# Kernel tuning notes

Measured on AMD Instinct MI355X. Metric: run time of the kernel, lower is better.

The kernel has to match this reference:

```python
import jax, jax.numpy as jnp
import numpy as np

CLAMP_MIN = 1e-12
CLAMP_MAX = 1e12


def setup_inputs() -> dict:
    key = jax.random.key(0)
    k1, k2, k3 = jax.random.split(key, 3)
    B, C, D = 16384, 751, 2048
    x = jax.random.normal(k1, (B, D), dtype=jnp.float32)
    labels = jax.random.randint(k2, (B,), 0, C, dtype=jnp.int64)
    centers = jax.random.normal(k3, (C, D), dtype=jnp.float32)
    return {"x": x, "labels": labels, "centers": centers}


def reference(x, labels, centers):
    # Original builds a full (B, C) squared-distance matrix and then, per row,
    # boolean-masks out the entry at column labels[i]. Mathematically that is
    # just the squared distance between x[i] and centers[labels[i]]; gradients
    # also only flow through those gathered entries, so we gather directly.
    c = centers[labels]                       # (B, D) own-class centers
    dist = (jnp.sum(x * x, axis=1)
            + jnp.sum(c * c, axis=1)
            - 2.0 * jnp.sum(x * c, axis=1))   # (B,) squared distances
    dist = jnp.clip(dist, CLAMP_MIN, CLAMP_MAX)
    return jnp.mean(dist)
```

## Files before the change

kernel.cpp:

```cpp
#include <hip/hip_runtime.h>

constexpr int B = 16384;
constexpr int D = 2048;
constexpr float CLAMP_MIN = 1e-12f;
constexpr float CLAMP_MAX = 1e12f;

constexpr int GRID1  = 2048;
constexpr int BLOCK1 = 256;

__global__ __launch_bounds__(BLOCK1) void center_loss_pass1(
    const float* __restrict__ x,
    const int* __restrict__ labels,
    const float* __restrict__ centers,
    float* __restrict__ partials)
{
    const int lane            = threadIdx.x & 63;
    const int wave_in_block   = threadIdx.x >> 6;
    const int waves_per_block = BLOCK1 >> 6;
    const int global_wave     = blockIdx.x * waves_per_block + wave_in_block;
    const int num_waves       = GRID1 * waves_per_block;

    float acc = 0.0f;

    for (int row = global_wave; row < B; row += num_waves) {
        const int lbl = __builtin_amdgcn_readfirstlane(labels[row]);
        const float4* __restrict__ xr =
            reinterpret_cast<const float4*>(x + (size_t)row * D);
        const float4* __restrict__ cr =
            reinterpret_cast<const float4*>(centers + (size_t)lbl * D);

        float partial = 0.0f;
        #pragma unroll
        for (int j = 0; j < D / 4 / 64; ++j) {
            float4 xv = xr[j * 64 + lane];
            float4 cv = cr[j * 64 + lane];
            float d0 = xv.x - cv.x;
            float d1 = xv.y - cv.y;
            float d2 = xv.z - cv.z;
            float d3 = xv.w - cv.w;
            partial = fmaf(d0, d0,
                      fmaf(d1, d1,
                      fmaf(d2, d2,
                      fmaf(d3, d3, partial))));
        }

        #pragma unroll
        for (int off = 32; off > 0; off >>= 1)
            partial += __shfl_xor(partial, off, 64);

        if (lane == 0) {
            acc += fminf(fmaxf(partial, CLAMP_MIN), CLAMP_MAX);
        }
    }

    __shared__ float s[4];
    if (lane == 0) s[wave_in_block] = acc;
    __syncthreads();
    if (threadIdx.x == 0) {
        partials[blockIdx.x] = (s[0] + s[1]) + (s[2] + s[3]);
    }
}

__global__ __launch_bounds__(256) void center_loss_pass2(
    const float* __restrict__ partials,
    float* __restrict__ out)
{
    const int tid = threadIdx.x;
    float v = 0.0f;
    #pragma unroll
    for (int j = 0; j < GRID1 / 256; ++j)
        v += partials[j * 256 + tid];

    #pragma unroll
    for (int off = 32; off > 0; off >>= 1)
        v += __shfl_xor(v, off, 64);

    __shared__ float s[4];
    if ((tid & 63) == 0) s[tid >> 6] = v;
    __syncthreads();
    if (tid == 0)
        out[0] = ((s[0] + s[1]) + (s[2] + s[3])) * (1.0f / (float)B);
}

extern "C" void kernel_launch(void* const* d_in, const int* in_sizes, int n_in,
                              void* d_out, int out_size, void* d_ws, size_t ws_size,
                              hipStream_t stream) {
    const float* x       = (const float*)d_in[0];
    const int*   labels  = (const int*)d_in[1];
    const float* centers = (const float*)d_in[2];
    float*       out     = (float*)d_out;
    float*       partials = (float*)d_ws;

    center_loss_pass1<<<GRID1, BLOCK1, 0, stream>>>(x, labels, centers, partials);
    center_loss_pass2<<<1, 256, 0, stream>>>(partials, out);
}
```

Before: 194.5 us.

## Fuse two-pass reduction into one cooperative kernel with grid sync

Merges the partial-sum kernel and the final reduction kernel into one cooperative launch that uses a grid-wide barrier, removing the second kernel launch. It halves the grid to 1024 blocks so all blocks can be co-resident, and marks x loads as nontemporal so the streamed data does not evict reused center rows from cache. The cost is grid-sync overhead and fewer waves available to hide memory latency.

```diff
diff --git a/kernel.cpp b/kernel.cpp
--- a/kernel.cpp
+++ b/kernel.cpp
@@ -1,18 +1,24 @@
 #include <hip/hip_runtime.h>
+#include <hip/hip_cooperative_groups.h>
+
+namespace cg = cooperative_groups;
 
 constexpr int B = 16384;
 constexpr int D = 2048;
 constexpr float CLAMP_MIN = 1e-12f;
 constexpr float CLAMP_MAX = 1e12f;
 
-constexpr int GRID1  = 2048;
+constexpr int GRID1  = 1024;
 constexpr int BLOCK1 = 256;
 
-__global__ __launch_bounds__(BLOCK1) void center_loss_pass1(
+typedef float vfloat4 __attribute__((ext_vector_type(4)));
+
+__global__ __launch_bounds__(BLOCK1, 4) void center_loss_coop(
     const float* __restrict__ x,
     const int* __restrict__ labels,
     const float* __restrict__ centers,
-    float* __restrict__ partials)
+    float* __restrict__ partials,
+    float* __restrict__ out)
 {
     const int lane            = threadIdx.x & 63;
     const int wave_in_block   = threadIdx.x >> 6;
@@ -24,16 +30,16 @@
 
     for (int row = global_wave; row < B; row += num_waves) {
         const int lbl = __builtin_amdgcn_readfirstlane(labels[row]);
-        const float4* __restrict__ xr =
-            reinterpret_cast<const float4*>(x + (size_t)row * D);
-        const float4* __restrict__ cr =
-            reinterpret_cast<const float4*>(centers + (size_t)lbl * D);
+        const vfloat4* __restrict__ xr =
+            reinterpret_cast<const vfloat4*>(x + (size_t)row * D);
+        const vfloat4* __restrict__ cr =
+            reinterpret_cast<const vfloat4*>(centers + (size_t)lbl * D);
 
         float partial = 0.0f;
         #pragma unroll
         for (int j = 0; j < D / 4 / 64; ++j) {
-            float4 xv = xr[j * 64 + lane];
-            float4 cv = cr[j * 64 + lane];
+            vfloat4 xv = __builtin_nontemporal_load(&xr[j * 64 + lane]);
+            vfloat4 cv = cr[j * 64 + lane];
             float d0 = xv.x - cv.x;
             float d1 = xv.y - cv.y;
             float d2 = xv.z - cv.z;
@@ -56,41 +62,41 @@
     __shared__ float s[4];
     if (lane == 0) s[wave_in_block] = acc;
     __syncthreads();
-    if (threadIdx.x == 0) {
+    if (threadIdx.x == 0)
         partials[blockIdx.x] = (s[0] + s[1]) + (s[2] + s[3]);
+
+    cg::this_grid().sync();
+
+    if (blockIdx.x == 0) {
+        const int tid = threadIdx.x;
+        float v = 0.0f;
+        #pragma unroll
+        for (int j = 0; j < GRID1 / BLOCK1; ++j)
+            v += partials[j * BLOCK1 + tid];
+
+        #pragma unroll
+        for (int off = 32; off > 0; off >>= 1)
+            v += __shfl_xor(v, off, 64);
+
+        __shared__ float s2[4];
+        if ((tid & 63) == 0) s2[tid >> 6] = v;
+        __syncthreads();
+        if (tid == 0)
+            out[0] = ((s2[0] + s2[1]) + (s2[2] + s2[3])) * (1.0f / (float)B);
     }
-}
-
-__global__ __launch_bounds__(256) void center_loss_pass2(
-    const float* __restrict__ partials,
-    float* __restrict__ out)
-{
-    const int tid = threadIdx.x;
-    float v = 0.0f;
-    #pragma unroll
-    for (int j = 0; j < GRID1 / 256; ++j)
-        v += partials[j * 256 + tid];
-
-    #pragma unroll
-    for (int off = 32; off > 0; off >>= 1)
-        v += __shfl_xor(v, off, 64);
-
-    __shared__ float s[4];
-    if ((tid & 63) == 0) s[tid >> 6] = v;
-    __syncthreads();
-    if (tid == 0)
-        out[0] = ((s[0] + s[1]) + (s[2] + s[3])) * (1.0f / (float)B);
 }
 
 extern "C" void kernel_launch(void* const* d_in, const int* in_sizes, int n_in,
                               void* d_out, int out_size, void* d_ws, size_t ws_size,
                               hipStream_t stream) {
-    const float* x       = (const float*)d_in[0];
-    const int*   labels  = (const int*)d_in[1];
-    const float* centers = (const float*)d_in[2];
-    float*       out     = (float*)d_out;
+    const float* x        = (const float*)d_in[0];
+    const int*   labels   = (const int*)d_in[1];
+    const float* centers  = (const float*)d_in[2];
+    float*       out      = (float*)d_out;
     float*       partials = (float*)d_ws;
 
-    center_loss_pass1<<<GRID1, BLOCK1, 0, stream>>>(x, labels, centers, partials);
-    center_loss_pass2<<<1, 256, 0, stream>>>(partials, out);
+    void* args[] = {(void*)&x, (void*)&labels, (void*)&centers,
+                    (void*)&partials, (void*)&out};
+    (void)hipLaunchCooperativeKernel((const void*)center_loss_coop,
+                                     dim3(GRID1), dim3(BLOCK1), args, 0, stream);
 }
```

Measured after the change: 316.7 us. 62.8% more time.
